# Optimization experiments

Measured on AMD Instinct MI355X. Metric: run time of the kernel, lower is better.

The kernel has to match this reference:

```python
import jax, jax.numpy as jnp
import numpy as np

N_NODES = 100000
N_EDGES = 1600000
D_IN = 64
D_H = 64
N_CLS = 2


def setup_inputs() -> dict:
    key = jax.random.key(0)
    ks = jax.random.split(key, 12)
    s = 0.05
    return {
        "features": jax.random.normal(ks[0], (N_NODES, D_IN), dtype=jnp.float32),
        "edge_index": jax.random.randint(ks[1], (2, N_EDGES), 0, N_NODES, dtype=jnp.int64),
        # SAGE layer 1: Linear(2*D_IN, D_H)
        "W1": jax.random.normal(ks[2], (D_H, 2 * D_IN), dtype=jnp.float32) * s,
        "b1": jnp.zeros((D_H,), dtype=jnp.float32),
        # SAGE layer 2: Linear(2*D_H, D_H)
        "W2": jax.random.normal(ks[3], (D_H, 2 * D_H), dtype=jnp.float32) * s,
        "b2": jnp.zeros((D_H,), dtype=jnp.float32),
        # classifier: Linear(D_H, D_H//2) -> ReLU -> Linear(D_H//2, N_CLS)
        "Wc1": jax.random.normal(ks[4], (D_H // 2, D_H), dtype=jnp.float32) * s,
        "bc1": jnp.zeros((D_H // 2,), dtype=jnp.float32),
        "Wc2": jax.random.normal(ks[5], (N_CLS, D_H // 2), dtype=jnp.float32) * s,
        "bc2": jnp.zeros((N_CLS,), dtype=jnp.float32),
    }


def _sage_layer(x, edge_index, W, b):
    # gather src features, scatter-mean into dst, concat with self, linear
    src, dst = edge_index[0], edge_index[1]
    n = x.shape[0]
    ones = jnp.ones(src.shape[0], dtype=x.dtype)
    deg = jax.ops.segment_sum(ones, dst, num_segments=n)
    deg = jnp.maximum(deg, 1.0)  # clamp(min=1)
    neigh = jax.ops.segment_sum(x[src], dst, num_segments=n) / deg[:, None]
    combined = jnp.concatenate([x, neigh], axis=-1)  # [n, 2*d]
    return combined @ W.T + b


def reference(features, edge_index, W1, b1, W2, b2, Wc1, bc1, Wc2, bc2):
    # two SAGE layers with ReLU (dropout = identity at eval)
    x = jax.nn.relu(_sage_layer(features, edge_index, W1, b1))
    x = jax.nn.relu(_sage_layer(x, edge_index, W2, b2))
    # classifier head (embedding_projection unused when return_embeddings=False)
    h = jax.nn.relu(x @ Wc1.T + bc1)
    logits = h @ Wc2.T + bc2
    return logits
```

## Files before the change

### kernel.cpp

```cpp
#include <hip/hip_runtime.h>

#define D 64
#define TSCAN 1024
#define NB_SCAN 98

__device__ __forceinline__ float bcast(float v, int l) {
    return __uint_as_float(__builtin_amdgcn_readlane(__float_as_uint(v), l));
}

__global__ void __launch_bounds__(256) hist_kernel(
    const int* __restrict__ dst, int* __restrict__ cnt, int E)
{
    int t = blockIdx.x * blockDim.x + threadIdx.x;
    int st = gridDim.x * blockDim.x;
    for (int e = t; e < E; e += st) atomicAdd(&cnt[dst[e]], 1);
}

__global__ void __launch_bounds__(TSCAN) partial_kernel(
    const int* __restrict__ cnt, int* __restrict__ partials, int n)
{
    __shared__ int red[TSCAN];
    int i = blockIdx.x * TSCAN + threadIdx.x;
    red[threadIdx.x] = (i < n) ? cnt[i] : 0;
    __syncthreads();
    for (int off = TSCAN / 2; off > 0; off >>= 1) {
        if (threadIdx.x < off) red[threadIdx.x] += red[threadIdx.x + off];
        __syncthreads();
    }
    if (threadIdx.x == 0) partials[blockIdx.x] = red[0];
}

__global__ void __launch_bounds__(128) scanp_kernel(
    const int* __restrict__ partials, int* __restrict__ blockoff, int nb)
{
    __shared__ int s[128];
    int t = threadIdx.x;
    int orig = (t < nb) ? partials[t] : 0;
    s[t] = orig;
    __syncthreads();
    for (int off = 1; off < 128; off <<= 1) {
        int v = (t >= off) ? s[t - off] : 0;
        __syncthreads();
        s[t] += v;
        __syncthreads();
    }
    if (t < nb) blockoff[t] = s[t] - orig;
}

__global__ void __launch_bounds__(TSCAN) rowptr_kernel(
    const int* __restrict__ cnt, const int* __restrict__ blockoff,
    int* __restrict__ rowptr, int* __restrict__ cursor, int n)
{
    __shared__ int s[TSCAN];
    int b = blockIdx.x;
    int i = b * TSCAN + threadIdx.x;
    int v = (i < n) ? cnt[i] : 0;
    s[threadIdx.x] = v;
    __syncthreads();
    for (int off = 1; off < TSCAN; off <<= 1) {
        int x = (threadIdx.x >= off) ? s[threadIdx.x - off] : 0;
        __syncthreads();
        s[threadIdx.x] += x;
        __syncthreads();
    }
    if (i < n) {
        int excl = blockoff[b] + s[threadIdx.x] - v;
        rowptr[i] = excl;
        cursor[i] = excl;
        if (i == n - 1) rowptr[n] = excl + v;
    }
}

__global__ void __launch_bounds__(256) fill_kernel(
    const int* __restrict__ src, const int* __restrict__ dst,
    int* __restrict__ cursor, int* __restrict__ adj, int E)
{
    int t = blockIdx.x * blockDim.x + threadIdx.x;
    int st = gridDim.x * blockDim.x;
    for (int e = t; e < E; e += st) {
        int p = atomicAdd(&cursor[dst[e]], 1);
        adj[p] = src[e];
    }
}

template <bool HEAD>
__global__ void __launch_bounds__(512) sage_kernel(
    const float* __restrict__ x,
    const int*   __restrict__ rowptr,
    const int*   __restrict__ adj,
    const float* __restrict__ W,
    const float* __restrict__ b,
    const float* __restrict__ Wc1,
    const float* __restrict__ bc1,
    const float* __restrict__ Wc2,
    const float* __restrict__ bc2,
    float*       __restrict__ out,
    int n)
{
    extern __shared__ float smem[];
    float4* Wt4 = (float4*)smem;
    float*  Wt  = smem;
    float*  bs  = smem + 8192;
    float*  wc1t = bs + 64;
    float*  w2s  = wc1t + 2048;
    float*  bc1s = w2s + 64;
    float*  bc2s = bc1s + 32;

    for (int i = threadIdx.x; i < 64 * 128; i += blockDim.x) {
        int j = i >> 7, k = i & 127;
        Wt[(k >> 2) * 256 + j * 4 + (k & 3)] = W[i];
    }
    if (threadIdx.x < 64) bs[threadIdx.x] = b[threadIdx.x];
    if (HEAD) {
        for (int i = threadIdx.x; i < 32 * 64; i += blockDim.x) {
            int l = i >> 6, k = i & 63;
            wc1t[k * 32 + l] = Wc1[i];
        }
        if (threadIdx.x < 64) w2s[threadIdx.x] = Wc2[threadIdx.x];
        if (threadIdx.x < 32) bc1s[threadIdx.x] = bc1[threadIdx.x];
        if (threadIdx.x < 2)  bc2s[threadIdx.x] = bc2[threadIdx.x];
    }
    __syncthreads();

    int lane = threadIdx.x & 63;
    int wid  = (blockIdx.x * blockDim.x + threadIdx.x) >> 6;
    int nw   = (gridDim.x * blockDim.x) >> 6;
    for (int node = wid; node < n; node += nw) {
        int ro = rowptr[node], re = rowptr[node + 1];
        float acc = 0.f;
        int i = ro;
        for (; i + 4 <= re; i += 4) {
            int s0 = adj[i + 0], s1 = adj[i + 1], s2 = adj[i + 2], s3 = adj[i + 3];
            float v0 = x[(size_t)s0 * D + lane];
            float v1 = x[(size_t)s1 * D + lane];
            float v2 = x[(size_t)s2 * D + lane];
            float v3 = x[(size_t)s3 * D + lane];
            acc += (v0 + v1) + (v2 + v3);
        }
        for (; i < re; ++i) acc += x[(size_t)adj[i] * D + lane];
        float av = acc / fmaxf((float)(re - ro), 1.0f);
        float xv = x[(size_t)node * D + lane];

        float sum = bs[lane];
        #pragma unroll
        for (int k4 = 0; k4 < 16; ++k4) {
            float4 w = Wt4[k4 * 64 + lane];
            sum = fmaf(bcast(xv, 4 * k4 + 0), w.x, sum);
            sum = fmaf(bcast(xv, 4 * k4 + 1), w.y, sum);
            sum = fmaf(bcast(xv, 4 * k4 + 2), w.z, sum);
            sum = fmaf(bcast(xv, 4 * k4 + 3), w.w, sum);
        }
        #pragma unroll
        for (int k4 = 16; k4 < 32; ++k4) {
            float4 w = Wt4[k4 * 64 + lane];
            int kk = 4 * (k4 - 16);
            sum = fmaf(bcast(av, kk + 0), w.x, sum);
            sum = fmaf(bcast(av, kk + 1), w.y, sum);
            sum = fmaf(bcast(av, kk + 2), w.z, sum);
            sum = fmaf(bcast(av, kk + 3), w.w, sum);
        }
        float x2 = fmaxf(sum, 0.0f);

        if (!HEAD) {
            out[(size_t)node * D + lane] = x2;
        } else {
            int l = lane & 31;
            float h = bc1s[l];
            #pragma unroll
            for (int k = 0; k < 64; ++k)
                h = fmaf(bcast(x2, k), wc1t[k * 32 + l], h);
            h = fmaxf(h, 0.0f);
            float p0 = (lane < 32) ? h * w2s[l]      : 0.0f;
            float p1 = (lane < 32) ? h * w2s[32 + l] : 0.0f;
            #pragma unroll
            for (int off = 1; off < 64; off <<= 1) {
                p0 += __shfl_xor(p0, off, 64);
                p1 += __shfl_xor(p1, off, 64);
            }
            if (lane == 0) {
                out[(size_t)node * 2 + 0] = p0 + bc2s[0];
                out[(size_t)node * 2 + 1] = p1 + bc2s[1];
            }
        }
    }
}

extern "C" void kernel_launch(void* const* d_in, const int* in_sizes, int n_in,
                              void* d_out, int out_size, void* d_ws, size_t ws_size,
                              hipStream_t stream)
{
    const float* feat = (const float*)d_in[0];
    const int*   eidx = (const int*)d_in[1];
    const float* W1   = (const float*)d_in[2];
    const float* b1   = (const float*)d_in[3];
    const float* W2   = (const float*)d_in[4];
    const float* b2   = (const float*)d_in[5];
    const float* Wc1  = (const float*)d_in[6];
    const float* bc1  = (const float*)d_in[7];
    const float* Wc2  = (const float*)d_in[8];
    const float* bc2  = (const float*)d_in[9];

    int n = in_sizes[0] / D;
    int E = in_sizes[1] / 2;
    const int* src = eidx;
    const int* dst = eidx + E;

    int*   cnt      = (int*)d_ws;
    int*   partials = cnt + n;
    int*   blockoff = partials + 128;
    int*   rowptr   = blockoff + 128;
    int*   cursor   = rowptr + n + 1;
    int*   adj      = cursor + n;
    float* x1       = (float*)(adj + E);

    int nb = (n + TSCAN - 1) / TSCAN;

    hipMemsetAsync(cnt, 0, (size_t)n * sizeof(int), stream);
    hist_kernel<<<6250, 256, 0, stream>>>(dst, cnt, E);
    partial_kernel<<<nb, TSCAN, 0, stream>>>(cnt, partials, n);
    scanp_kernel<<<1, 128, 0, stream>>>(partials, blockoff, nb);
    rowptr_kernel<<<nb, TSCAN, 0, stream>>>(cnt, blockoff, rowptr, cursor, n);
    fill_kernel<<<6250, 256, 0, stream>>>(src, dst, cursor, adj, E);

    size_t lds1 = (8192 + 64) * sizeof(float);
    sage_kernel<false><<<12500, 512, lds1, stream>>>(
        feat, rowptr, adj, W1, b1, nullptr, nullptr, nullptr, nullptr, x1, n);

    size_t lds2 = (8192 + 64 + 2048 + 64 + 32 + 2) * sizeof(float);
    sage_kernel<true><<<12500, 512, lds2, stream>>>(
        x1, rowptr, adj, W2, b2, Wc1, bc1, Wc2, bc2, (float*)d_out, n);
}
```

Measured before the change: 983.5 us.

## Use persistent grid for SAGE kernels, unroll gather by 8, coalesce weight staging

The SAGE kernels now launch 512 persistent blocks with a min-blocks-per-CU hint instead of 12500 blocks. This amortises the per-block LDS weight staging, which otherwise runs once per 8 nodes. The neighbour gather loop is unrolled to 8 loads with two accumulators to keep more memory requests in flight. Weight transposition now writes LDS contiguously and reads global memory strided. The small grid may underfill the GPU or lose latency hiding, and the higher unroll raises register pressure.

```diff
diff --git a/kernel.cpp b/kernel.cpp
--- a/kernel.cpp
+++ b/kernel.cpp
@@ -2,7 +2,6 @@
 
 #define D 64
 #define TSCAN 1024
-#define NB_SCAN 98
 
 __device__ __forceinline__ float bcast(float v, int l) {
     return __uint_as_float(__builtin_amdgcn_readlane(__float_as_uint(v), l));
@@ -84,7 +83,7 @@
 }
 
 template <bool HEAD>
-__global__ void __launch_bounds__(512) sage_kernel(
+__global__ void __launch_bounds__(512, 4) sage_kernel(
     const float* __restrict__ x,
     const int*   __restrict__ rowptr,
     const int*   __restrict__ adj,
@@ -106,15 +105,17 @@
     float*  bc1s = w2s + 64;
     float*  bc2s = bc1s + 32;
 
-    for (int i = threadIdx.x; i < 64 * 128; i += blockDim.x) {
-        int j = i >> 7, k = i & 127;
-        Wt[(k >> 2) * 256 + j * 4 + (k & 3)] = W[i];
+    for (int d = threadIdx.x; d < 64 * 128; d += blockDim.x) {
+        int k4 = d >> 8;
+        int j  = (d >> 2) & 63;
+        int kk = d & 3;
+        Wt[d] = W[j * 128 + k4 * 4 + kk];
     }
     if (threadIdx.x < 64) bs[threadIdx.x] = b[threadIdx.x];
     if (HEAD) {
-        for (int i = threadIdx.x; i < 32 * 64; i += blockDim.x) {
-            int l = i >> 6, k = i & 63;
-            wc1t[k * 32 + l] = Wc1[i];
+        for (int d = threadIdx.x; d < 32 * 64; d += blockDim.x) {
+            int k = d >> 5, l = d & 31;
+            wc1t[d] = Wc1[l * 64 + k];
         }
         if (threadIdx.x < 64) w2s[threadIdx.x] = Wc2[threadIdx.x];
         if (threadIdx.x < 32) bc1s[threadIdx.x] = bc1[threadIdx.x];
@@ -127,17 +128,24 @@
     int nw   = (gridDim.x * blockDim.x) >> 6;
     for (int node = wid; node < n; node += nw) {
         int ro = rowptr[node], re = rowptr[node + 1];
-        float acc = 0.f;
+        float acc0 = 0.f, acc1 = 0.f;
         int i = ro;
-        for (; i + 4 <= re; i += 4) {
-            int s0 = adj[i + 0], s1 = adj[i + 1], s2 = adj[i + 2], s3 = adj[i + 3];
+        for (; i + 8 <= re; i += 8) {
+            int s0 = adj[i+0], s1 = adj[i+1], s2 = adj[i+2], s3 = adj[i+3];
+            int s4 = adj[i+4], s5 = adj[i+5], s6 = adj[i+6], s7 = adj[i+7];
             float v0 = x[(size_t)s0 * D + lane];
             float v1 = x[(size_t)s1 * D + lane];
             float v2 = x[(size_t)s2 * D + lane];
             float v3 = x[(size_t)s3 * D + lane];
-            acc += (v0 + v1) + (v2 + v3);
-        }
-        for (; i < re; ++i) acc += x[(size_t)adj[i] * D + lane];
+            float v4 = x[(size_t)s4 * D + lane];
+            float v5 = x[(size_t)s5 * D + lane];
+            float v6 = x[(size_t)s6 * D + lane];
+            float v7 = x[(size_t)s7 * D + lane];
+            acc0 += (v0 + v1) + (v2 + v3);
+            acc1 += (v4 + v5) + (v6 + v7);
+        }
+        for (; i < re; ++i) acc0 += x[(size_t)adj[i] * D + lane];
+        float acc = acc0 + acc1;
         float av = acc / fmaxf((float)(re - ro), 1.0f);
         float xv = x[(size_t)node * D + lane];
 
@@ -223,10 +231,10 @@
     fill_kernel<<<6250, 256, 0, stream>>>(src, dst, cursor, adj, E);
 
     size_t lds1 = (8192 + 64) * sizeof(float);
-    sage_kernel<false><<<12500, 512, lds1, stream>>>(
+    sage_kernel<false><<<512, 512, lds1, stream>>>(
         feat, rowptr, adj, W1, b1, nullptr, nullptr, nullptr, nullptr, x1, n);
 
     size_t lds2 = (8192 + 64 + 2048 + 64 + 32 + 2) * sizeof(float);
-    sage_kernel<true><<<12500, 512, lds2, stream>>>(
+    sage_kernel<true><<<512, 512, lds2, stream>>>(
         x1, rowptr, adj, W2, b2, Wc1, bc1, Wc2, bc2, (float*)d_out, n);
 }
```

Result: faster. 917.7 us (-6.7%).
